# Kernel tuning notes

Measured on AMD Instinct MI355X. Metric: run time of the kernel, lower is better.

Reference implementation:

```python
import math
import jax, jax.numpy as jnp
import numpy as np

DIM = 256
HEADS = 8
WS = (8, 8)   # window_size
SS = (4, 4)   # shift_size


def _rel_tables():
    """Static SwinV2 continuous relative-position coordinate table and index."""
    wh, ww = WS
    ch = np.arange(-(wh - 1), wh, dtype=np.float32)
    cw = np.arange(-(ww - 1), ww, dtype=np.float32)
    table = np.stack(np.meshgrid(ch, cw, indexing='ij'), axis=-1)  # (2wh-1, 2ww-1, 2)
    table[..., 0] /= (wh - 1)
    table[..., 1] /= (ww - 1)
    table *= 8.0
    table = np.sign(table) * np.log2(np.abs(table) + 1.0) / 3.0
    coords = np.stack(np.meshgrid(np.arange(wh), np.arange(ww), indexing='ij'))
    cf = coords.reshape(2, -1)                      # (2, N)
    rel = (cf[:, :, None] - cf[:, None, :]).transpose(1, 2, 0)  # (N, N, 2)
    rel[..., 0] += wh - 1
    rel[..., 1] += ww - 1
    rel[..., 0] *= 2 * ww - 1
    idx = rel.sum(-1).reshape(-1)                   # (N*N,)
    return jnp.asarray(table, jnp.float32), jnp.asarray(idx, jnp.int32)


def _attn_mask(pad_H, pad_W, sh, sw):
    """Static shifted-window attention mask, shape (num_windows, N, N)."""
    wh, ww = WS
    m = np.zeros((pad_H, pad_W), np.float32)
    cnt = 0
    for hs in ((0, -wh), (-wh, -sh), (-sh, None)):
        for ws_ in ((0, -ww), (-ww, -sw), (-sw, None)):
            m[hs[0]:hs[1], ws_[0]:ws_[1]] = cnt
            cnt += 1
    m = m.reshape(pad_H // wh, wh, pad_W // ww, ww).transpose(0, 2, 1, 3)
    m = m.reshape(-1, wh * ww)                      # (nW, N)
    diff = m[:, None, :] - m[:, :, None]            # (nW, N, N)
    return jnp.asarray(np.where(diff != 0, -100.0, 0.0).astype(np.float32))


def setup_inputs() -> dict:
    key = jax.random.key(0)
    ks = jax.random.split(key, 12)
    C, Hh = DIM, HEADS
    s = 0.02
    inp = {
        'x': jax.random.normal(ks[0], (16, 64, 64, C), jnp.float32),
        'Wq': jax.random.normal(ks[1], (C, C), jnp.float32) * s,
        'bq': jnp.zeros((C,), jnp.float32),
        'Wk': jax.random.normal(ks[2], (C, C), jnp.float32) * s,
        'bk': jnp.zeros((C,), jnp.float32),
        'Wv': jax.random.normal(ks[3], (C, C), jnp.float32) * s,
        'bv': jnp.zeros((C,), jnp.float32),
        'Wo': jax.random.normal(ks[4], (C, C), jnp.float32) * s,
        'bo': jnp.zeros((C,), jnp.float32),
        'logit_scale': jnp.full((Hh, 1, 1), math.log(10.0), jnp.float32),
        'cpb_w1': jax.random.normal(ks[5], (2, 512), jnp.float32) * s,
        'cpb_b1': jnp.zeros((512,), jnp.float32),
        'cpb_w2': jax.random.normal(ks[6], (512, Hh), jnp.float32) * s,
    }
    return inp


def reference(x, Wq, bq, Wk, bk, Wv, bv, Wo, bo, logit_scale, cpb_w1, cpb_b1, cpb_w2):
    B, H, W, C = x.shape
    wh, ww = WS
    hd = C // HEADS
    pad_b = (wh - H % wh) % wh
    pad_r = (ww - W % ww) % ww
    x = jnp.pad(x, ((0, 0), (0, pad_b), (0, pad_r), (0, 0)))
    pH, pW = H + pad_b, W + pad_r
    sh = 0 if wh >= pH else SS[0]
    sw = 0 if ww >= pW else SS[1]

    xs = jnp.roll(x, (-sh, -sw), axis=(1, 2))
    nW = (pH // wh) * (pW // ww)
    N = wh * ww
    # window partition -> (B*nW, N, C)
    xw = xs.reshape(B, pH // wh, wh, pW // ww, ww, C).transpose(0, 1, 3, 2, 4, 5)
    xw = xw.reshape(B * nW, N, C)

    def heads(t):
        return t.reshape(B * nW, N, HEADS, hd).transpose(0, 2, 1, 3)  # (BnW, H, N, hd)

    q = heads(xw @ Wq + bq)
    k = heads(xw @ Wk + bk)
    v = heads(xw @ Wv + bv)

    # cosine attention (F.normalize, eps=1e-12)
    qn = q / jnp.maximum(jnp.linalg.norm(q, axis=-1, keepdims=True), 1e-12)
    kn = k / jnp.maximum(jnp.linalg.norm(k, axis=-1, keepdims=True), 1e-12)
    attn = jnp.einsum('bhnd,bhmd->bhnm', qn, kn)

    scale = jnp.exp(jnp.minimum(logit_scale, math.log(100.0)))  # (HEADS,1,1)
    attn = attn * scale[None]

    table, idx = _rel_tables()
    bias = jax.nn.relu(table @ cpb_w1 + cpb_b1) @ cpb_w2        # (2wh-1, 2ww-1, HEADS)
    bias = bias.reshape(-1, HEADS)[idx].reshape(N, N, HEADS).transpose(2, 0, 1)
    attn = attn + (16.0 * jax.nn.sigmoid(bias))[None]

    if sh + sw > 0:
        mask = _attn_mask(pH, pW, sh, sw)                        # (nW, N, N)
        attn = attn.reshape(B, nW, HEADS, N, N) + mask[None, :, None]
        attn = attn.reshape(B * nW, HEADS, N, N)

    attn = jax.nn.softmax(attn, axis=-1)
    out = jnp.einsum('bhnm,bhmd->bhnd', attn, v)
    out = out.transpose(0, 2, 1, 3).reshape(B * nW, N, C)
    out = out @ Wo + bo

    out = out.reshape(B, pH // wh, pW // ww, wh, ww, C).transpose(0, 1, 3, 2, 4, 5)
    out = out.reshape(B, pH, pW, C)
    if sh + sw > 0:
        out = jnp.roll(out, (sh, sw), axis=(1, 2))
    return out[:, :H, :W, :]
```

## Files before the change

kernel.cpp:

```cpp
#include <hip/hip_runtime.h>
#include <hip/hip_bf16.h>

typedef float floatx4 __attribute__((ext_vector_type(4)));
typedef short shortx8 __attribute__((ext_vector_type(8)));
typedef short shortx4 __attribute__((ext_vector_type(4)));

#define CFENCE() asm volatile("" ::: "memory")

__device__ __forceinline__ float bf2f(short s) {
    union { unsigned u; float f; } cv;
    cv.u = ((unsigned)(unsigned short)s) << 16;
    return cv.f;
}
__device__ __forceinline__ short f2bf(float f) {
    union { float f; unsigned u; } cv; cv.f = f;
    unsigned r = (cv.u + 0x7fffu + ((cv.u >> 16) & 1u)) >> 16;
    return (short)r;
}

__global__ __launch_bounds__(256) void wtrans(const float* __restrict__ Wq,
                                              const float* __restrict__ Wk,
                                              const float* __restrict__ Wv,
                                              const float* __restrict__ Wo,
                                              short* __restrict__ wqkv_f,
                                              short* __restrict__ wo_f) {
    int gtid = blockIdx.x * 256 + threadIdx.x;
    int f = gtid >> 6, lane = gtid & 63;
    int quad = lane >> 4, l15 = lane & 15;
    if (f < 384) {
        int n16 = f >> 3, kt = f & 7;
        int n = n16 * 16 + l15, z = n >> 8, ncol = n & 255;
        const float* src = (z == 0) ? Wq : (z == 1) ? Wk : Wv;
        shortx8 s;
#pragma unroll
        for (int j = 0; j < 8; ++j)
            s[j] = f2bf(src[(size_t)(kt * 32 + quad * 8 + j) * 256 + ncol]);
        *(shortx8*)(wqkv_f + (size_t)f * 512 + lane * 8) = s;
    } else {
        int f2 = f - 384;
        int n16 = f2 >> 3, kt = f2 & 7;
        int n = n16 * 16 + l15;
        shortx8 s;
#pragma unroll
        for (int j = 0; j < 8; ++j)
            s[j] = f2bf(Wo[(size_t)(kt * 32 + quad * 8 + j) * 256 + n]);
        *(shortx8*)(wo_f + (size_t)f2 * 512 + lane * 8) = s;
    }
}

__device__ __forceinline__ float sgnlog(float x) {
    return copysignf(__log2f(fabsf(x) + 1.f) / 3.f, x);
}
__global__ __launch_bounds__(256) void bias_mlp(const float* __restrict__ ls,
                                                const float* __restrict__ w1,
                                                const float* __restrict__ b1,
                                                const float* __restrict__ w2,
                                                float* __restrict__ b225g,
                                                float* __restrict__ scaleOut) {
    int e = blockIdx.x;
    int tid = threadIdx.x, lane = tid & 63, wid = tid >> 6;
    if (e == 0 && tid < 8) scaleOut[tid] = expf(fminf(ls[tid], 4.6051701859880914f));
    int dh = e / 15 - 7, dw = e % 15 - 7;
    float t0 = sgnlog(8.f * (float)dh / 7.f);
    float t1 = sgnlog(8.f * (float)dw / 7.f);
    float acc[8];
#pragma unroll
    for (int j = 0; j < 8; ++j) acc[j] = 0.f;
#pragma unroll
    for (int s = 0; s < 2; ++s) {
        int hsm = tid + s * 256;
        float hid = fmaxf(0.f, t0 * w1[hsm] + t1 * w1[512 + hsm] + b1[hsm]);
#pragma unroll
        for (int j = 0; j < 8; ++j) acc[j] += hid * w2[hsm * 8 + j];
    }
#pragma unroll
    for (int off = 1; off < 64; off <<= 1)
#pragma unroll
        for (int j = 0; j < 8; ++j) acc[j] += __shfl_xor(acc[j], off, 64);
    __shared__ float red[4][8];
    if (lane == 0)
#pragma unroll
        for (int j = 0; j < 8; ++j) red[wid][j] = acc[j];
    __syncthreads();
    if (tid < 8)
        b225g[e * 8 + tid] = red[0][tid] + red[1][tid] + red[2][tid] + red[3][tid];
}

__global__ __launch_bounds__(256) void bias_expand(const float* __restrict__ b225g,
                                                   float* __restrict__ bias_t) {
    int f = blockIdx.x * 256 + threadIdx.x;
    int h = f >> 12, ij = f & 4095, i = ij >> 6, j = ij & 63;
    int dh = (i >> 3) - (j >> 3), dw = (i & 7) - (j & 7);
    int e = (dh + 7) * 15 + (dw + 7);
    float v = b225g[e * 8 + h];
    bias_t[(h << 12) + j * 64 + i] = 16.f / (1.f + expf(-v));
}

__device__ __forceinline__ int row2pix(int row) {
    int w = row >> 6, t = row & 63;
    int b = w >> 6, wi = (w >> 3) & 7, wj = w & 7;
    int hh = (wi * 8 + (t >> 3) + 4) & 63;
    int ww = (wj * 8 + (t & 7) + 4) & 63;
    return (b * 64 + hh) * 64 + ww;
}

__device__ __forceinline__ int regid(int t, int wi, int wj) {
    int a = (wi < 7) ? 0 : (((t >> 3) < 4) ? 1 : 2);
    int b = (wj < 7) ? 0 : (((t & 7) < 4) ? 1 : 2);
    return a * 3 + b;
}

__global__ __launch_bounds__(512, 2) void swin_fused(const float* __restrict__ x,
                                                     const short* __restrict__ wf,
                                                     const short* __restrict__ wof,
                                                     const float* __restrict__ bq,
                                                     const float* __restrict__ bk_,
                                                     const float* __restrict__ bv,
                                                     const float* __restrict__ bo,
                                                     const float* __restrict__ bias_t,
                                                     const float* __restrict__ scale,
                                                     float* __restrict__ out) {
    __shared__ __align__(16) short lds[68608];
    int tid = threadIdx.x, lane = tid & 63, wid = tid >> 6;
    int quad = lane >> 4, l15 = lane & 15;
    int win = blockIdx.x;
    int wi = (win >> 3) & 7, wj = win & 7;
    bool need_mask = (wi == 7) || (wj == 7);

    short* xtile = lds;
    short* qn = &lds[16384 + wid * 6528];
    short* kn = qn + 2176;
    short* vt = qn + 4352;
    short* P  = qn;

    {
        int r = tid >> 3, seg = tid & 7;
        const float* src = x + (size_t)row2pix(win * 64 + r) * 256 + seg * 32;
        short* dst = &xtile[((r >> 4) * 8 + seg) * 512 + (r & 15) * 8];
#pragma unroll
        for (int c4 = 0; c4 < 4; ++c4) {
            float4 u0 = *(const float4*)(src + c4 * 8);
            float4 u1 = *(const float4*)(src + c4 * 8 + 4);
            shortx8 t;
            t[0] = f2bf(u0.x); t[1] = f2bf(u0.y); t[2] = f2bf(u0.z); t[3] = f2bf(u0.w);
            t[4] = f2bf(u1.x); t[5] = f2bf(u1.y); t[6] = f2bf(u1.z); t[7] = f2bf(u1.w);
            *(shortx8*)(dst + c4 * 128) = t;
        }
    }
    __syncthreads();

    int h = wid;
    float sc = scale[h];

    floatx4 aq[2][4], ak[2][4];
#pragma unroll
    for (int i = 0; i < 2; ++i)
#pragma unroll
        for (int mt = 0; mt < 4; ++mt) {
            aq[i][mt] = (floatx4){0.f, 0.f, 0.f, 0.f};
            ak[i][mt] = (floatx4){0.f, 0.f, 0.f, 0.f};
        }
#pragma unroll
    for (int kt = 0; kt < 8; ++kt) {
        shortx8 af[4];
#pragma unroll
        for (int mt = 0; mt < 4; ++mt)
            af[mt] = *(const shortx8*)&xtile[(mt * 8 + kt) * 512 + lane * 8];
        shortx8 wqf[2], wkf[2];
#pragma unroll
        for (int i = 0; i < 2; ++i) {
            int n16 = 2 * h + i;
            wqf[i] = *(const shortx8*)(wf + (size_t)((n16)*8 + kt) * 512 + lane * 8);
            wkf[i] = *(const shortx8*)(wf + (size_t)((16 + n16) * 8 + kt) * 512 + lane * 8);
        }
#pragma unroll
        for (int i = 0; i < 2; ++i)
#pragma unroll
            for (int mt = 0; mt < 4; ++mt) {
                aq[i][mt] = __builtin_amdgcn_mfma_f32_16x16x32_bf16(wqf[i], af[mt], aq[i][mt], 0, 0, 0);
                ak[i][mt] = __builtin_amdgcn_mfma_f32_16x16x32_bf16(wkf[i], af[mt], ak[i][mt], 0, 0, 0);
            }
    }
    float qs[4], ks[4];
#pragma unroll
    for (int mt = 0; mt < 4; ++mt) { qs[mt] = 0.f; ks[mt] = 0.f; }
#pragma unroll
    for (int i = 0; i < 2; ++i) {
        float bqv[4], bkv[4];
#pragma unroll
        for (int r = 0; r < 4; ++r) {
            int d = i * 16 + quad * 4 + r;
            bqv[r] = bq[h * 32 + d];
            bkv[r] = bk_[h * 32 + d];
        }
#pragma unroll
        for (int mt = 0; mt < 4; ++mt)
#pragma unroll
            for (int r = 0; r < 4; ++r) {
                float qv = aq[i][mt][r] + bqv[r]; aq[i][mt][r] = qv; qs[mt] += qv * qv;
                float kv = ak[i][mt][r] + bkv[r]; ak[i][mt][r] = kv; ks[mt] += kv * kv;
            }
    }
#pragma unroll
    for (int mt = 0; mt < 4; ++mt) {
        qs[mt] += __shfl_xor(qs[mt], 16, 64); qs[mt] += __shfl_xor(qs[mt], 32, 64);
        ks[mt] += __shfl_xor(ks[mt], 16, 64); ks[mt] += __shfl_xor(ks[mt], 32, 64);
    }
    CFENCE();
#pragma unroll
    for (int mt = 0; mt < 4; ++mt) {
        float qr = sc / fmaxf(sqrtf(qs[mt]), 1e-12f);
        float kr = 1.f / fmaxf(sqrtf(ks[mt]), 1e-12f);
        int tok = mt * 16 + l15;
#pragma unroll
        for (int i = 0; i < 2; ++i) {
            shortx4 oq, ok;
#pragma unroll
            for (int r = 0; r < 4; ++r) {
                oq[r] = f2bf(aq[i][mt][r] * qr);
                ok[r] = f2bf(ak[i][mt][r] * kr);
            }
            *(shortx4*)&qn[tok * 34 + i * 16 + quad * 4] = oq;
            *(shortx4*)&kn[tok * 34 + i * 16 + quad * 4] = ok;
        }
    }
    CFENCE();
    floatx4 av[2][4];
#pragma unroll
    for (int i = 0; i < 2; ++i)
#pragma unroll
        for (int mt = 0; mt < 4; ++mt) av[i][mt] = (floatx4){0.f, 0.f, 0.f, 0.f};
#pragma unroll
    for (int kt = 0; kt < 8; ++kt) {
        shortx8 af[4];
#pragma unroll
        for (int mt = 0; mt < 4; ++mt)
            af[mt] = *(const shortx8*)&xtile[(mt * 8 + kt) * 512 + lane * 8];
        shortx8 wvf[2];
#pragma unroll
        for (int i = 0; i < 2; ++i) {
            int n16 = 2 * h + i;
            wvf[i] = *(const shortx8*)(wf + (size_t)((32 + n16) * 8 + kt) * 512 + lane * 8);
        }
#pragma unroll
        for (int i = 0; i < 2; ++i)
#pragma unroll
            for (int mt = 0; mt < 4; ++mt)
                av[i][mt] = __builtin_amdgcn_mfma_f32_16x16x32_bf16(wvf[i], af[mt], av[i][mt], 0, 0, 0);
    }
#pragma unroll
    for (int i = 0; i < 2; ++i) {
        float bvv[4];
#pragma unroll
        for (int r = 0; r < 4; ++r) bvv[r] = bv[h * 32 + i * 16 + quad * 4 + r];
#pragma unroll
        for (int mt = 0; mt < 4; ++mt) {
            int tok = mt * 16 + l15;
#pragma unroll
            for (int r = 0; r < 4; ++r)
                vt[(i * 16 + quad * 4 + r) * 68 + tok] = f2bf(av[i][mt][r] + bvv[r]);
        }
    }
    CFENCE();
    shortx8 aqf[4], bkf[4];
#pragma unroll
    for (int mt = 0; mt < 4; ++mt)
        aqf[mt] = *(const shortx8*)&qn[(mt * 16 + l15) * 34 + quad * 8];
#pragma unroll
    for (int nt = 0; nt < 4; ++nt)
        bkf[nt] = *(const shortx8*)&kn[(nt * 16 + l15) * 34 + quad * 8];
    floatx4 S[4][4];
#pragma unroll
    for (int mt = 0; mt < 4; ++mt)
#pragma unroll
        for (int nt = 0; nt < 4; ++nt) {
            floatx4 z = {0.f, 0.f, 0.f, 0.f};
            S[mt][nt] = __builtin_amdgcn_mfma_f32_16x16x32_bf16(aqf[mt], bkf[nt], z, 0, 0, 0);
        }
    const float* bh = bias_t + (h << 12);
    float bound = sc + 16.5f;
    int jid[4];
    if (need_mask) {
#pragma unroll
        for (int nt = 0; nt < 4; ++nt) jid[nt] = regid(nt * 16 + l15, wi, wj);
    }
    float rs[4][4];
#pragma unroll
    for (int mt = 0; mt < 4; ++mt) {
        float4 b4[4];
#pragma unroll
        for (int nt = 0; nt < 4; ++nt)
            b4[nt] = *(const float4*)&bh[(nt * 16 + l15) * 64 + mt * 16 + quad * 4];
#pragma unroll
        for (int reg = 0; reg < 4; ++reg) {
            int i = mt * 16 + quad * 4 + reg;
            int iid = need_mask ? regid(i, wi, wj) : 0;
            float rowsum = 0.f;
#pragma unroll
            for (int nt = 0; nt < 4; ++nt) {
                float bb = (reg == 0) ? b4[nt].x : (reg == 1) ? b4[nt].y
                         : (reg == 2) ? b4[nt].z : b4[nt].w;
                float v = S[mt][nt][reg] + bb;
                if (need_mask && iid != jid[nt]) v -= 100.f;
                float pe = __expf(v - bound);
                S[mt][nt][reg] = pe;
                rowsum += pe;
            }
            rowsum += __shfl_xor(rowsum, 1, 64);
            rowsum += __shfl_xor(rowsum, 2, 64);
            rowsum += __shfl_xor(rowsum, 4, 64);
            rowsum += __shfl_xor(rowsum, 8, 64);
            rs[mt][reg] = 1.f / rowsum;
        }
    }
    CFENCE();
#pragma unroll
    for (int mt = 0; mt < 4; ++mt)
#pragma unroll
        for (int nt = 0; nt < 4; ++nt)
#pragma unroll
            for (int reg = 0; reg < 4; ++reg)
                P[(mt * 16 + quad * 4 + reg) * 68 + nt * 16 + l15] = f2bf(S[mt][nt][reg]);
    CFENCE();
    floatx4 O[4][2];
#pragma unroll
    for (int mt = 0; mt < 4; ++mt)
#pragma unroll
        for (int nt = 0; nt < 2; ++nt) O[mt][nt] = (floatx4){0.f, 0.f, 0.f, 0.f};
#pragma unroll
    for (int ks2 = 0; ks2 < 2; ++ks2) {
        shortx8 pa[4], vb[2];
#pragma unroll
        for (int mt = 0; mt < 4; ++mt)
            pa[mt] = *(const shortx8*)&P[(mt * 16 + l15) * 68 + ks2 * 32 + quad * 8];
#pragma unroll
        for (int nt = 0; nt < 2; ++nt)
            vb[nt] = *(const shortx8*)&vt[(nt * 16 + l15) * 68 + ks2 * 32 + quad * 8];
#pragma unroll
        for (int mt = 0; mt < 4; ++mt)
#pragma unroll
            for (int nt = 0; nt < 2; ++nt)
                O[mt][nt] = __builtin_amdgcn_mfma_f32_16x16x32_bf16(pa[mt], vb[nt], O[mt][nt], 0, 0, 0);
    }
    shortx4 Obf[4][2];
#pragma unroll
    for (int mt = 0; mt < 4; ++mt)
#pragma unroll
        for (int nt = 0; nt < 2; ++nt) {
            shortx4 s;
#pragma unroll
            for (int reg = 0; reg < 4; ++reg)
                s[reg] = f2bf(O[mt][nt][reg] * rs[mt][reg]);
            Obf[mt][nt] = s;
        }

    __syncthreads();
    short* Ao = lds;
#pragma unroll
    for (int mt = 0; mt < 4; ++mt)
#pragma unroll
        for (int nt = 0; nt < 2; ++nt)
#pragma unroll
            for (int reg = 0; reg < 4; ++reg)
                Ao[(mt * 16 + quad * 4 + reg) * 264 + h * 32 + nt * 16 + l15] =
                    Obf[mt][nt][reg];
    __syncthreads();

    int pix[4];
#pragma unroll
    for (int mt = 0; mt < 4; ++mt) pix[mt] = row2pix(win * 64 + mt * 16 + l15);

    floatx4 acc2[2][4];
#pragma unroll
    for (int nt = 0; nt < 2; ++nt)
#pragma unroll
        for (int mt = 0; mt < 4; ++mt) acc2[nt][mt] = (floatx4){0.f, 0.f, 0.f, 0.f};
#pragma unroll
    for (int kt = 0; kt < 8; ++kt) {
        shortx8 bw[2], af2[4];
#pragma unroll
        for (int nt = 0; nt < 2; ++nt)
            bw[nt] = *(const shortx8*)(wof + (size_t)((wid * 2 + nt) * 8 + kt) * 512 + lane * 8);
#pragma unroll
        for (int mt = 0; mt < 4; ++mt)
            af2[mt] = *(const shortx8*)&Ao[(mt * 16 + l15) * 264 + kt * 32 + quad * 8];
#pragma unroll
        for (int nt = 0; nt < 2; ++nt)
#pragma unroll
            for (int mt = 0; mt < 4; ++mt)
                acc2[nt][mt] = __builtin_amdgcn_mfma_f32_16x16x32_bf16(bw[nt], af2[mt], acc2[nt][mt], 0, 0, 0);
    }
#pragma unroll
    for (int nt = 0; nt < 2; ++nt) {
        int nb = (wid * 2 + nt) * 16 + quad * 4;
        float bs[4];
#pragma unroll
        for (int reg = 0; reg < 4; ++reg) bs[reg] = bo[nb + reg];
#pragma unroll
        for (int mt = 0; mt < 4; ++mt) {
            float4 o;
            o.x = acc2[nt][mt][0] + bs[0];
            o.y = acc2[nt][mt][1] + bs[1];
            o.z = acc2[nt][mt][2] + bs[2];
            o.w = acc2[nt][mt][3] + bs[3];
            *(float4*)(out + (size_t)pix[mt] * 256 + nb) = o;
        }
    }
}

extern "C" void kernel_launch(void* const* d_in, const int* in_sizes, int n_in,
                              void* d_out, int out_size, void* d_ws, size_t ws_size,
                              hipStream_t stream) {
    const float* x  = (const float*)d_in[0];
    const float* Wq = (const float*)d_in[1];
    const float* bq = (const float*)d_in[2];
    const float* Wk = (const float*)d_in[3];
    const float* bk = (const float*)d_in[4];
    const float* Wv = (const float*)d_in[5];
    const float* bv = (const float*)d_in[6];
    const float* Wo = (const float*)d_in[7];
    const float* bo = (const float*)d_in[8];
    const float* ls = (const float*)d_in[9];
    const float* w1 = (const float*)d_in[10];
    const float* b1 = (const float*)d_in[11];
    const float* w2 = (const float*)d_in[12];

    char* ws = (char*)d_ws;
    short* wqkv_f = (short*)(ws + 0);
    short* wo_f   = (short*)(ws + 393216);
    float* bias_t = (float*)(ws + 524288);
    float* scale  = (float*)(ws + 655360);
    float* b225g  = (float*)(ws + 786432);
    float* out    = (float*)d_out;

    hipLaunchKernelGGL(wtrans, dim3(128), dim3(256), 0, stream, Wq, Wk, Wv, Wo, wqkv_f, wo_f);
    hipLaunchKernelGGL(bias_mlp, dim3(225), dim3(256), 0, stream, ls, w1, b1, w2, b225g, scale);
    hipLaunchKernelGGL(bias_expand, dim3(128), dim3(256), 0, stream, b225g, bias_t);
    hipLaunchKernelGGL(swin_fused, dim3(1024), dim3(512), 0, stream,
                       x, wqkv_f, wo_f, bq, bk, bv, bo, bias_t, scale, out);
}
```

Measured before the change: 225.9 us.

## Swizzle x tile in LDS, transpose score tile, add MFMA priority hints

Stores the bf16 x tile with an XOR swizzle on the row-within-fragment index so the strided fragment reads spread across LDS banks. Computes the score tile transposed (K times Q), so each query row sits in a lane column and its softmax row sum needs only two cross-lane shuffles instead of four per row. Normalisation moves from the output accumulator onto P before it is written to LDS. The bias table is stored untransposed to match, and s_setprio hints are placed around the MFMA loops. The added swizzle index arithmetic and the new P store pattern could themselves cause bank conflicts.

Measured after the change: 220.7 us. 1.02x faster.

```diff
diff --git a/kernel.cpp b/kernel.cpp
--- a/kernel.cpp
+++ b/kernel.cpp
@@ -87,13 +87,13 @@
 }
 
 __global__ __launch_bounds__(256) void bias_expand(const float* __restrict__ b225g,
-                                                   float* __restrict__ bias_t) {
+                                                   float* __restrict__ bias8) {
     int f = blockIdx.x * 256 + threadIdx.x;
     int h = f >> 12, ij = f & 4095, i = ij >> 6, j = ij & 63;
     int dh = (i >> 3) - (j >> 3), dw = (i & 7) - (j & 7);
     int e = (dh + 7) * 15 + (dw + 7);
     float v = b225g[e * 8 + h];
-    bias_t[(h << 12) + j * 64 + i] = 16.f / (1.f + expf(-v));
+    bias8[f] = 16.f / (1.f + expf(-v));
 }
 
 __device__ __forceinline__ int row2pix(int row) {
@@ -117,7 +117,7 @@
                                                      const float* __restrict__ bk_,
                                                      const float* __restrict__ bv,
                                                      const float* __restrict__ bo,
-                                                     const float* __restrict__ bias_t,
+                                                     const float* __restrict__ bias8,
                                                      const float* __restrict__ scale,
                                                      float* __restrict__ out) {
     __shared__ __align__(16) short lds[68608];
@@ -136,7 +136,8 @@
     {
         int r = tid >> 3, seg = tid & 7;
         const float* src = x + (size_t)row2pix(win * 64 + r) * 256 + seg * 32;
-        short* dst = &xtile[((r >> 4) * 8 + seg) * 512 + (r & 15) * 8];
+        short* fbase = &xtile[((r >> 4) * 8 + seg) * 512];
+        int slo = (r & 15) ^ seg;
 #pragma unroll
         for (int c4 = 0; c4 < 4; ++c4) {
             float4 u0 = *(const float4*)(src + c4 * 8);
@@ -144,7 +145,7 @@
             shortx8 t;
             t[0] = f2bf(u0.x); t[1] = f2bf(u0.y); t[2] = f2bf(u0.z); t[3] = f2bf(u0.w);
             t[4] = f2bf(u1.x); t[5] = f2bf(u1.y); t[6] = f2bf(u1.z); t[7] = f2bf(u1.w);
-            *(shortx8*)(dst + c4 * 128) = t;
+            *(shortx8*)(fbase + (c4 * 16 + slo) * 8) = t;
         }
     }
     __syncthreads();
@@ -165,7 +166,7 @@
         shortx8 af[4];
 #pragma unroll
         for (int mt = 0; mt < 4; ++mt)
-            af[mt] = *(const shortx8*)&xtile[(mt * 8 + kt) * 512 + lane * 8];
+            af[mt] = *(const shortx8*)&xtile[(mt * 8 + kt) * 512 + (lane ^ kt) * 8];
         shortx8 wqf[2], wkf[2];
 #pragma unroll
         for (int i = 0; i < 2; ++i) {
@@ -173,6 +174,7 @@
             wqf[i] = *(const shortx8*)(wf + (size_t)((n16)*8 + kt) * 512 + lane * 8);
             wkf[i] = *(const shortx8*)(wf + (size_t)((16 + n16) * 8 + kt) * 512 + lane * 8);
         }
+        __builtin_amdgcn_s_setprio(1);
 #pragma unroll
         for (int i = 0; i < 2; ++i)
 #pragma unroll
@@ -180,6 +182,7 @@
                 aq[i][mt] = __builtin_amdgcn_mfma_f32_16x16x32_bf16(wqf[i], af[mt], aq[i][mt], 0, 0, 0);
                 ak[i][mt] = __builtin_amdgcn_mfma_f32_16x16x32_bf16(wkf[i], af[mt], ak[i][mt], 0, 0, 0);
             }
+        __builtin_amdgcn_s_setprio(0);
     }
     float qs[4], ks[4];
 #pragma unroll
@@ -235,18 +238,20 @@
         shortx8 af[4];
 #pragma unroll
         for (int mt = 0; mt < 4; ++mt)
-            af[mt] = *(const shortx8*)&xtile[(mt * 8 + kt) * 512 + lane * 8];
+            af[mt] = *(const shortx8*)&xtile[(mt * 8 + kt) * 512 + (lane ^ kt) * 8];
         shortx8 wvf[2];
 #pragma unroll
         for (int i = 0; i < 2; ++i) {
             int n16 = 2 * h + i;
             wvf[i] = *(const shortx8*)(wf + (size_t)((32 + n16) * 8 + kt) * 512 + lane * 8);
         }
+        __builtin_amdgcn_s_setprio(1);
 #pragma unroll
         for (int i = 0; i < 2; ++i)
 #pragma unroll
             for (int mt = 0; mt < 4; ++mt)
                 av[i][mt] = __builtin_amdgcn_mfma_f32_16x16x32_bf16(wvf[i], af[mt], av[i][mt], 0, 0, 0);
+        __builtin_amdgcn_s_setprio(0);
     }
 #pragma unroll
     for (int i = 0; i < 2; ++i) {
@@ -275,52 +280,53 @@
 #pragma unroll
         for (int nt = 0; nt < 4; ++nt) {
             floatx4 z = {0.f, 0.f, 0.f, 0.f};
-            S[mt][nt] = __builtin_amdgcn_mfma_f32_16x16x32_bf16(aqf[mt], bkf[nt], z, 0, 0, 0);
-        }
-    const float* bh = bias_t + (h << 12);
+            S[mt][nt] = __builtin_amdgcn_mfma_f32_16x16x32_bf16(bkf[mt], aqf[nt], z, 0, 0, 0);
+        }
+    const float* bh = bias8 + (h << 12);
     float bound = sc + 16.5f;
-    int jid[4];
+    int jd[4][4];
     if (need_mask) {
 #pragma unroll
-        for (int nt = 0; nt < 4; ++nt) jid[nt] = regid(nt * 16 + l15, wi, wj);
-    }
-    float rs[4][4];
-#pragma unroll
-    for (int mt = 0; mt < 4; ++mt) {
-        float4 b4[4];
-#pragma unroll
-        for (int nt = 0; nt < 4; ++nt)
-            b4[nt] = *(const float4*)&bh[(nt * 16 + l15) * 64 + mt * 16 + quad * 4];
-#pragma unroll
-        for (int reg = 0; reg < 4; ++reg) {
-            int i = mt * 16 + quad * 4 + reg;
-            int iid = need_mask ? regid(i, wi, wj) : 0;
-            float rowsum = 0.f;
-#pragma unroll
-            for (int nt = 0; nt < 4; ++nt) {
-                float bb = (reg == 0) ? b4[nt].x : (reg == 1) ? b4[nt].y
-                         : (reg == 2) ? b4[nt].z : b4[nt].w;
+        for (int mt = 0; mt < 4; ++mt)
+#pragma unroll
+            for (int reg = 0; reg < 4; ++reg)
+                jd[mt][reg] = regid(mt * 16 + quad * 4 + reg, wi, wj);
+    }
+    float rsinv[4];
+#pragma unroll
+    for (int nt = 0; nt < 4; ++nt) {
+        int qt = nt * 16 + l15;
+        int iid = need_mask ? regid(qt, wi, wj) : 0;
+        const float* brow = bh + qt * 64;
+        float rowsum = 0.f;
+#pragma unroll
+        for (int mt = 0; mt < 4; ++mt) {
+            float4 b4 = *(const float4*)&brow[mt * 16 + quad * 4];
+#pragma unroll
+            for (int reg = 0; reg < 4; ++reg) {
+                float bb = (reg == 0) ? b4.x : (reg == 1) ? b4.y : (reg == 2) ? b4.z : b4.w;
                 float v = S[mt][nt][reg] + bb;
-                if (need_mask && iid != jid[nt]) v -= 100.f;
+                if (need_mask && iid != jd[mt][reg]) v -= 100.f;
                 float pe = __expf(v - bound);
                 S[mt][nt][reg] = pe;
                 rowsum += pe;
             }
-            rowsum += __shfl_xor(rowsum, 1, 64);
-            rowsum += __shfl_xor(rowsum, 2, 64);
-            rowsum += __shfl_xor(rowsum, 4, 64);
-            rowsum += __shfl_xor(rowsum, 8, 64);
-            rs[mt][reg] = 1.f / rowsum;
-        }
+        }
+        rowsum += __shfl_xor(rowsum, 16, 64);
+        rowsum += __shfl_xor(rowsum, 32, 64);
+        rsinv[nt] = 1.f / rowsum;
     }
     CFENCE();
 #pragma unroll
-    for (int mt = 0; mt < 4; ++mt)
-#pragma unroll
-        for (int nt = 0; nt < 4; ++nt)
+    for (int nt = 0; nt < 4; ++nt)
+#pragma unroll
+        for (int mt = 0; mt < 4; ++mt) {
+            shortx4 s;
 #pragma unroll
             for (int reg = 0; reg < 4; ++reg)
-                P[(mt * 16 + quad * 4 + reg) * 68 + nt * 16 + l15] = f2bf(S[mt][nt][reg]);
+                s[reg] = f2bf(S[mt][nt][reg] * rsinv[nt]);
+            *(shortx4*)&P[(nt * 16 + l15) * 68 + mt * 16 + quad * 4] = s;
+        }
     CFENCE();
     floatx4 O[4][2];
 #pragma unroll
@@ -350,7 +356,7 @@
             shortx4 s;
 #pragma unroll
             for (int reg = 0; reg < 4; ++reg)
-                s[reg] = f2bf(O[mt][nt][reg] * rs[mt][reg]);
+                s[reg] = f2bf(O[mt][nt][reg]);
             Obf[mt][nt] = s;
         }
 
@@ -384,11 +390,13 @@
 #pragma unroll
         for (int mt = 0; mt < 4; ++mt)
             af2[mt] = *(const shortx8*)&Ao[(mt * 16 + l15) * 264 + kt * 32 + quad * 8];
+        __builtin_amdgcn_s_setprio(1);
 #pragma unroll
         for (int nt = 0; nt < 2; ++nt)
 #pragma unroll
             for (int mt = 0; mt < 4; ++mt)
                 acc2[nt][mt] = __builtin_amdgcn_mfma_f32_16x16x32_bf16(bw[nt], af2[mt], acc2[nt][mt], 0, 0, 0);
+        __builtin_amdgcn_s_setprio(0);
     }
 #pragma unroll
     for (int nt = 0; nt < 2; ++nt) {
@@ -428,14 +436,14 @@
     char* ws = (char*)d_ws;
     short* wqkv_f = (short*)(ws + 0);
     short* wo_f   = (short*)(ws + 393216);
-    float* bias_t = (float*)(ws + 524288);
+    float* bias8  = (float*)(ws + 524288);
     float* scale  = (float*)(ws + 655360);
     float* b225g  = (float*)(ws + 786432);
     float* out    = (float*)d_out;
 
     hipLaunchKernelGGL(wtrans, dim3(128), dim3(256), 0, stream, Wq, Wk, Wv, Wo, wqkv_f, wo_f);
     hipLaunchKernelGGL(bias_mlp, dim3(225), dim3(256), 0, stream, ls, w1, b1, w2, b225g, scale);
-    hipLaunchKernelGGL(bias_expand, dim3(128), dim3(256), 0, stream, b225g, bias_t);
+    hipLaunchKernelGGL(bias_expand, dim3(128), dim3(256), 0, stream, b225g, bias8);
     hipLaunchKernelGGL(swin_fused, dim3(1024), dim3(512), 0, stream,
-                       x, wqkv_f, wo_f, bq, bk, bv, bo, bias_t, scale, out);
-}
+                       x, wqkv_f, wo_f, bq, bk, bv, bo, bias8, scale, out);
+}
```
